# Kernel tuning notes

Measured on AMD Instinct MI355X. Metric: run time of the kernel, lower is better.

Reference implementation:

```python
import jax, jax.numpy as jnp
import numpy as np

N = 50000      # nodes
E = 800000     # random edges (self-loops appended -> E + N total)
IN = 128       # in_channels
H = 1          # heads
C = 128        # out_channels per head
NEG_SLOPE = 0.2


def setup_inputs() -> dict:
    key = jax.random.key(0)
    k1, k2, k3, k4, k5 = jax.random.split(key, 5)
    x = jax.random.normal(k1, (N, IN), jnp.float32)
    src = jax.random.randint(k2, (E,), 0, N)
    dst = jax.random.randint(k3, (E,), 0, N)
    loops = jnp.arange(N)
    # PyG 1.3.2 GATConv adds self-loops before propagate
    edge_index = jnp.stack([jnp.concatenate([src, loops]),
                            jnp.concatenate([dst, loops])]).astype(jnp.int64)
    W = jax.random.normal(k4, (IN, H * C), jnp.float32) * np.float32(1.0 / np.sqrt(IN))
    att = jax.random.normal(k5, (H, 2 * C), jnp.float32) * np.float32(0.1)
    bias = jnp.zeros((H * C,), jnp.float32)
    return {"x": x, "edge_index": edge_index, "W": W, "att": att, "bias": bias}


def reference(x, edge_index, W, att, bias):
    h = (x @ W).reshape(-1, H, C)            # [N,H,C] transformed features
    src, dst = edge_index[0], edge_index[1]  # j -> i
    hi = h[dst]                              # [Etot,H,C] x_i gather
    hj = h[src]                              # [Etot,H,C] x_j gather
    # alpha = sum(cat(x_i,x_j) * att, -1)
    alpha = (jnp.einsum('ehc,hc->eh', hi, att[:, :C])
             + jnp.einsum('ehc,hc->eh', hj, att[:, C:]))
    alpha = jax.nn.leaky_relu(alpha, NEG_SLOPE)
    # segment softmax over destination node (stable)
    m = jax.ops.segment_max(alpha, dst, num_segments=N)
    m = jnp.where(jnp.isfinite(m), m, 0.0)   # guard empty segments
    a = jnp.exp(alpha - m[dst])
    s = jax.ops.segment_sum(a, dst, num_segments=N)
    a = a / (s[dst] + 1e-16)
    # weighted scatter-add aggregation
    out = jax.ops.segment_sum(hj * a[:, :, None], dst, num_segments=N)  # [N,H,C]
    return out.reshape(-1, H * C) + bias
```

## Files before the change

kernel.cpp:

```cpp
#include <hip/hip_runtime.h>
#include <math.h>


constexpr int CH = 128;
constexpr int BNODES = 64;
constexpr int CAP = 2048;
constexpr int SCAP = 2560;
constexpr int NBMAX = 1024;
constexpr int SCHUNK = 8192;
constexpr int WTS = 136;
constexpr unsigned SENT = 0xFFFFFFFFu;

typedef __attribute__((ext_vector_type(8))) short bf16x8;
typedef __attribute__((ext_vector_type(4))) float f32x4;

static __device__ __forceinline__ unsigned short f2bf(float f) {
    unsigned u = __float_as_uint(f);
    unsigned r = (u + 0x7fffu + ((u >> 16) & 1u)) >> 16;
    return (unsigned short)r;
}

__global__ __launch_bounds__(256) void zero_kernel(int* __restrict__ p, int n) {
    int i = blockIdx.x * blockDim.x + threadIdx.x;
    if (i < n) p[i] = 0;
}

__global__ __launch_bounds__(256) void wt_kernel(const float* __restrict__ W,
                                                 unsigned short* __restrict__ WT) {
    const int T = blockIdx.x * 256 + threadIdx.x;
    const int k = T >> 4;
    const int n8 = (T & 15) * 8;
    const float4 a = *(const float4*)&W[k * CH + n8];
    const float4 b = *(const float4*)&W[k * CH + n8 + 4];
    WT[(n8 + 0) * WTS + k] = f2bf(a.x);
    WT[(n8 + 1) * WTS + k] = f2bf(a.y);
    WT[(n8 + 2) * WTS + k] = f2bf(a.z);
    WT[(n8 + 3) * WTS + k] = f2bf(a.w);
    WT[(n8 + 4) * WTS + k] = f2bf(b.x);
    WT[(n8 + 5) * WTS + k] = f2bf(b.y);
    WT[(n8 + 6) * WTS + k] = f2bf(b.z);
    WT[(n8 + 7) * WTS + k] = f2bf(b.w);
}

__global__ __launch_bounds__(256) void gemm_kernel(const float* __restrict__ x,
                                                   const unsigned short* __restrict__ WT,
                                                   const float* __restrict__ att,
                                                   unsigned short* __restrict__ hb,
                                                   float* __restrict__ ad,
                                                   float* __restrict__ as_, int n) {
    __shared__ unsigned short Wl[CH * WTS];
    const int tid = threadIdx.x;
    {
        const uint4* s = (const uint4*)WT;
        uint4* d = (uint4*)Wl;
        for (int i = tid; i < CH * WTS / 8; i += 256) d[i] = s[i];
    }
    __syncthreads();

    const int lane = tid & 63, wave = tid >> 6;
    const int m = lane & 15, quad = lane >> 4;
    const int row0 = blockIdx.x * 64 + wave * 16;
    const int row = min(row0 + m, n - 1);
    const float* xr = x + (size_t)row * CH;

    float4 a0[4], a1[4];
    #pragma unroll
    for (int t = 0; t < 4; ++t) {
        const int k0 = t * 32 + quad * 8;
        a0[t] = *(const float4*)&xr[k0];
        a1[t] = *(const float4*)&xr[k0 + 4];
    }
    bf16x8 afr[4];
    #pragma unroll
    for (int t = 0; t < 4; ++t) {
        afr[t][0] = (short)f2bf(a0[t].x); afr[t][1] = (short)f2bf(a0[t].y);
        afr[t][2] = (short)f2bf(a0[t].z); afr[t][3] = (short)f2bf(a0[t].w);
        afr[t][4] = (short)f2bf(a1[t].x); afr[t][5] = (short)f2bf(a1[t].y);
        afr[t][6] = (short)f2bf(a1[t].z); afr[t][7] = (short)f2bf(a1[t].w);
    }

    f32x4 acc[8] = {};
    #pragma unroll
    for (int t = 0; t < 4; ++t) {
        const int kb = t * 32 + quad * 8;
        #pragma unroll
        for (int nt = 0; nt < 8; ++nt) {
            const bf16x8 bfr = *(const bf16x8*)&Wl[(nt * 16 + m) * WTS + kb];
            acc[nt] = __builtin_amdgcn_mfma_f32_16x16x32_bf16(afr[t], bfr, acc[nt], 0, 0, 0);
        }
    }

    const int rbase = row0 + quad * 4;
    float pd[4] = {}, ps[4] = {};
    #pragma unroll
    for (int nt = 0; nt < 8; ++nt) {
        const int col = nt * 16 + m;
        const float atd = att[col], ats = att[CH + col];
        #pragma unroll
        for (int r = 0; r < 4; ++r) {
            pd[r] = fmaf(acc[nt][r], atd, pd[r]);
            ps[r] = fmaf(acc[nt][r], ats, ps[r]);
            const int rr = rbase + r;
            if (rr < n) hb[(size_t)rr * CH + col] = f2bf(acc[nt][r]);
        }
    }
    #pragma unroll
    for (int r = 0; r < 4; ++r) {
        #pragma unroll
        for (int off = 8; off >= 1; off >>= 1) {
            pd[r] += __shfl_xor(pd[r], off, 64);
            ps[r] += __shfl_xor(ps[r], off, 64);
        }
        const int rr = rbase + r;
        if (m == 0 && rr < n) { ad[rr] = pd[r]; as_[rr] = ps[r]; }
    }
}

__global__ __launch_bounds__(256) void scatter_kernel(const int* __restrict__ src,
                                                      const int* __restrict__ dst,
                                                      int* __restrict__ gcur,
                                                      unsigned* __restrict__ recs,
                                                      int etot, int nb) {
    __shared__ int hist[NBMAX];
    __shared__ int cur[NBMAX];
    __shared__ unsigned rbuf[SCHUNK];
    const int tid = threadIdx.x;
    const int e0 = blockIdx.x * SCHUNK;
    for (int t = tid; t < nb; t += 256) hist[t] = 0;
    __syncthreads();
    for (int i = tid; i < SCHUNK; i += 256) {
        const int e = e0 + i;
        if (e < etot) {
            const int d = dst[e];
            rbuf[i] = ((unsigned)d << 16) | (unsigned)src[e];
            atomicAdd(&hist[d >> 6], 1);
        }
    }
    __syncthreads();
    for (int t = tid; t < nb; t += 256) {
        const int h = hist[t];
        cur[t] = h ? atomicAdd(&gcur[t], h) : 0;
    }
    __syncthreads();
    for (int i = tid; i < SCHUNK; i += 256) {
        const int e = e0 + i;
        if (e < etot) {
            const unsigned r = rbuf[i];
            const int d = (int)(r >> 16);
            const int b = d >> 6;
            const int pos = atomicAdd(&cur[b], 1);
            if (pos < CAP)
                recs[(size_t)b * CAP + pos] = ((unsigned)(d & 63) << 16) | (r & 0xffffu);
        }
    }
}

__global__ __launch_bounds__(512) void aggregate_kernel(const unsigned char* __restrict__ hwb,
                                                        const float* __restrict__ ad,
                                                        const float* __restrict__ as_,
                                                        const int* __restrict__ gcur,
                                                        const unsigned* __restrict__ recs,
                                                        const float* __restrict__ bias,
                                                        float* __restrict__ out, int n) {
    __shared__ alignas(16) unsigned sorted[SCAP];
    __shared__ alignas(16) float alphas[SCAP];
    __shared__ int cnt[BNODES], ofs[BNODES], cur[BNODES];
    __shared__ int nEp_s;
    const int b = blockIdx.x;
    const int tid = threadIdx.x, lane = tid & 63, wid = tid >> 6;
    const unsigned* br = recs + (size_t)b * CAP;
    int nE = gcur[b]; if (nE > CAP) nE = CAP;
    unsigned* stash = (unsigned*)alphas;

    if (tid < BNODES) cnt[tid] = 0;
    __syncthreads();
    for (int i = tid; i < nE; i += 512) {
        const unsigned r = br[i];
        stash[i] = r;
        atomicAdd(&cnt[r >> 16], 1);
    }
    __syncthreads();
    if (wid == 0) {
        const int c = cnt[lane];
        const int cr = (c + 7) & ~7;
        int v = cr;
        #pragma unroll
        for (int off = 1; off < 64; off <<= 1) {
            const int u = __shfl_up(v, (unsigned)off, 64);
            if (lane >= off) v += u;
        }
        ofs[lane] = v - cr;
        cur[lane] = v - cr;
        if (lane == 63) nEp_s = v;
    }
    __syncthreads();
    const int nEp = nEp_s;
    for (int i = tid; i < nEp; i += 512) sorted[i] = SENT;
    __syncthreads();
    for (int i = tid; i < nE; i += 512) {
        const unsigned r = stash[i];
        const int pos = atomicAdd(&cur[r >> 16], 1);
        sorted[pos] = r;
    }
    __syncthreads();
    const float* adb = ad + b * BNODES;
    for (int i = tid; i < nEp; i += 512) {
        const unsigned r = sorted[i];
        float a = -3.0e38f;
        if (r != SENT) {
            a = adb[r >> 16] + as_[r & 0xffffu];
            a = (a >= 0.f) ? a : 0.2f * a;
        }
        alphas[i] = a;
    }
    __syncthreads();

    const unsigned lane4 = (unsigned)lane * 4u;
    for (int ln = wid; ln < BNODES; ln += 8) {
        const int node = b * BNODES + ln;
        if (node >= n) break;
        const int start = ofs[ln];
        const int endp = start + ((cnt[ln] + 7) & ~7);

        float m = -3.0e38f;
        for (int e = start + lane; e < endp; e += 64) m = fmaxf(m, alphas[e]);
        #pragma unroll
        for (int off = 32; off >= 1; off >>= 1) m = fmaxf(m, __shfl_xor(m, off, 64));

        float s = 0.f;
        for (int e = start + lane; e < endp; e += 64) {
            const float p = __expf(alphas[e] - m);
            alphas[e] = p;
            s += p;
            const unsigned r = sorted[e];
            sorted[e] = (r == SENT) ? 0u : ((r & 0xffffu) << 8);
        }
        #pragma unroll
        for (int off = 32; off >= 1; off >>= 1) s += __shfl_xor(s, off, 64);

        float acc0 = 0.f, acc1 = 0.f;
        for (int e = start; e < endp; e += 8) {
            const uint4 sa = *(const uint4*)&sorted[e];
            const uint4 sb = *(const uint4*)&sorted[e + 4];
            const float4 pa = *(const float4*)&alphas[e];
            const float4 pb = *(const float4*)&alphas[e + 4];
            const unsigned g0 = *(const unsigned*)(hwb + (sa.x + lane4));
            const unsigned g1 = *(const unsigned*)(hwb + (sa.y + lane4));
            const unsigned g2 = *(const unsigned*)(hwb + (sa.z + lane4));
            const unsigned g3 = *(const unsigned*)(hwb + (sa.w + lane4));
            const unsigned g4 = *(const unsigned*)(hwb + (sb.x + lane4));
            const unsigned g5 = *(const unsigned*)(hwb + (sb.y + lane4));
            const unsigned g6 = *(const unsigned*)(hwb + (sb.z + lane4));
            const unsigned g7 = *(const unsigned*)(hwb + (sb.w + lane4));
            acc0 = fmaf(pa.x, __uint_as_float((g0 & 0xffffu) << 16), acc0);
            acc1 = fmaf(pa.x, __uint_as_float(g0 & 0xffff0000u), acc1);
            acc0 = fmaf(pa.y, __uint_as_float((g1 & 0xffffu) << 16), acc0);
            acc1 = fmaf(pa.y, __uint_as_float(g1 & 0xffff0000u), acc1);
            acc0 = fmaf(pa.z, __uint_as_float((g2 & 0xffffu) << 16), acc0);
            acc1 = fmaf(pa.z, __uint_as_float(g2 & 0xffff0000u), acc1);
            acc0 = fmaf(pa.w, __uint_as_float((g3 & 0xffffu) << 16), acc0);
            acc1 = fmaf(pa.w, __uint_as_float(g3 & 0xffff0000u), acc1);
            acc0 = fmaf(pb.x, __uint_as_float((g4 & 0xffffu) << 16), acc0);
            acc1 = fmaf(pb.x, __uint_as_float(g4 & 0xffff0000u), acc1);
            acc0 = fmaf(pb.y, __uint_as_float((g5 & 0xffffu) << 16), acc0);
            acc1 = fmaf(pb.y, __uint_as_float(g5 & 0xffff0000u), acc1);
            acc0 = fmaf(pb.z, __uint_as_float((g6 & 0xffffu) << 16), acc0);
            acc1 = fmaf(pb.z, __uint_as_float(g6 & 0xffff0000u), acc1);
            acc0 = fmaf(pb.w, __uint_as_float((g7 & 0xffffu) << 16), acc0);
            acc1 = fmaf(pb.w, __uint_as_float(g7 & 0xffff0000u), acc1);
        }
        const float inv = 1.f / (s + 1e-16f);
        const float2 bv = *(const float2*)&bias[lane * 2];
        float2 o;
        o.x = fmaf(acc0, inv, bv.x);
        o.y = fmaf(acc1, inv, bv.y);
        *(float2*)&out[node * CH + lane * 2] = o;
    }
}

extern "C" void kernel_launch(void* const* d_in, const int* in_sizes, int n_in,
                              void* d_out, int out_size, void* d_ws, size_t ws_size,
                              hipStream_t stream) {
    const float* x    = (const float*)d_in[0];
    const int*   ei   = (const int*)d_in[1];
    const float* W    = (const float*)d_in[2];
    const float* att  = (const float*)d_in[3];
    const float* bias = (const float*)d_in[4];
    float* out = (float*)d_out;

    const int N_   = in_sizes[0] / CH;
    const int Etot = in_sizes[1] / 2;
    const int* src = ei;
    const int* dst = ei + Etot;
    const int nb = (N_ + BNODES - 1) / BNODES;

    char* ws = (char*)d_ws;
    size_t off = 0;
    auto alloc = [&](size_t bytes) -> void* {
        void* p = ws + off;
        off = (off + bytes + 255) & ~(size_t)255;
        return p;
    };
    unsigned short* hb = (unsigned short*)alloc((size_t)N_ * CH * sizeof(unsigned short));
    unsigned short* WT = (unsigned short*)alloc((size_t)CH * WTS * sizeof(unsigned short));
    float* ad      = (float*)alloc((size_t)N_ * sizeof(float));
    float* as_     = (float*)alloc((size_t)N_ * sizeof(float));
    int*   gcur    = (int*)  alloc((size_t)nb * sizeof(int));
    unsigned* recs = (unsigned*)alloc((size_t)nb * CAP * sizeof(unsigned));
    (void)ws_size; (void)n_in; (void)out_size;

    zero_kernel<<<(nb + 255) / 256, 256, 0, stream>>>(gcur, nb);
    wt_kernel<<<8, 256, 0, stream>>>(W, WT);
    gemm_kernel<<<(N_ + 63) / 64, 256, 0, stream>>>(x, WT, att, hb, ad, as_, N_);
    scatter_kernel<<<(Etot + SCHUNK - 1) / SCHUNK, 256, 0, stream>>>(src, dst, gcur, recs, Etot, nb);
    aggregate_kernel<<<nb, 512, 0, stream>>>((const unsigned char*)hb, ad, as_, gcur, recs, bias, out, N_);
}
```

Measured before the change: 153.1 us.

## Fuse zero into transpose kernel and run GEMM and scatter in one launch

Zeroing of the bucket counters moves into the weight-transpose kernel, and the GEMM and edge-scatter kernels are merged into one launch where block index selects the role. This removes two kernel launches and lets the independent GEMM and scatter work run concurrently on the GPU instead of back to back. The aggregate kernel also caches the per-block destination attention scores in shared memory. The cost is a shared 40 KB LDS allocation for every block, which can lower occupancy for the GEMM blocks. Correctness relies on the transpose grid covering all counters (8*256 >= nb).

Measured after the change: 144.5 us. 1.06x faster.

```diff
diff --git a/kernel.cpp b/kernel.cpp
--- a/kernel.cpp
+++ b/kernel.cpp
@@ -20,14 +20,11 @@
     return (unsigned short)r;
 }
 
-__global__ __launch_bounds__(256) void zero_kernel(int* __restrict__ p, int n) {
-    int i = blockIdx.x * blockDim.x + threadIdx.x;
-    if (i < n) p[i] = 0;
-}
-
-__global__ __launch_bounds__(256) void wt_kernel(const float* __restrict__ W,
-                                                 unsigned short* __restrict__ WT) {
+__global__ __launch_bounds__(256) void wtzero_kernel(const float* __restrict__ W,
+                                                     unsigned short* __restrict__ WT,
+                                                     int* __restrict__ gcur, int nb) {
     const int T = blockIdx.x * 256 + threadIdx.x;
+    if (T < nb) gcur[T] = 0;
     const int k = T >> 4;
     const int n8 = (T & 15) * 8;
     const float4 a = *(const float4*)&W[k * CH + n8];
@@ -42,115 +39,117 @@
     WT[(n8 + 7) * WTS + k] = f2bf(b.w);
 }
 
-__global__ __launch_bounds__(256) void gemm_kernel(const float* __restrict__ x,
-                                                   const unsigned short* __restrict__ WT,
-                                                   const float* __restrict__ att,
-                                                   unsigned short* __restrict__ hb,
-                                                   float* __restrict__ ad,
-                                                   float* __restrict__ as_, int n) {
-    __shared__ unsigned short Wl[CH * WTS];
+__global__ __launch_bounds__(256) void gemm_scatter_kernel(const float* __restrict__ x,
+                                                           const unsigned short* __restrict__ WT,
+                                                           const float* __restrict__ att,
+                                                           unsigned short* __restrict__ hb,
+                                                           float* __restrict__ ad,
+                                                           float* __restrict__ as_,
+                                                           const int* __restrict__ src,
+                                                           const int* __restrict__ dst,
+                                                           int* __restrict__ gcur,
+                                                           unsigned* __restrict__ recs,
+                                                           int n, int etot, int nb, int gb) {
+    __shared__ alignas(16) unsigned char smem[40960];
     const int tid = threadIdx.x;
-    {
-        const uint4* s = (const uint4*)WT;
-        uint4* d = (uint4*)Wl;
-        for (int i = tid; i < CH * WTS / 8; i += 256) d[i] = s[i];
-    }
-    __syncthreads();
-
-    const int lane = tid & 63, wave = tid >> 6;
-    const int m = lane & 15, quad = lane >> 4;
-    const int row0 = blockIdx.x * 64 + wave * 16;
-    const int row = min(row0 + m, n - 1);
-    const float* xr = x + (size_t)row * CH;
-
-    float4 a0[4], a1[4];
-    #pragma unroll
-    for (int t = 0; t < 4; ++t) {
-        const int k0 = t * 32 + quad * 8;
-        a0[t] = *(const float4*)&xr[k0];
-        a1[t] = *(const float4*)&xr[k0 + 4];
-    }
-    bf16x8 afr[4];
-    #pragma unroll
-    for (int t = 0; t < 4; ++t) {
-        afr[t][0] = (short)f2bf(a0[t].x); afr[t][1] = (short)f2bf(a0[t].y);
-        afr[t][2] = (short)f2bf(a0[t].z); afr[t][3] = (short)f2bf(a0[t].w);
-        afr[t][4] = (short)f2bf(a1[t].x); afr[t][5] = (short)f2bf(a1[t].y);
-        afr[t][6] = (short)f2bf(a1[t].z); afr[t][7] = (short)f2bf(a1[t].w);
-    }
-
-    f32x4 acc[8] = {};
-    #pragma unroll
-    for (int t = 0; t < 4; ++t) {
-        const int kb = t * 32 + quad * 8;
+
+    if ((int)blockIdx.x < gb) {
+        unsigned short* Wl = (unsigned short*)smem;
+        {
+            const uint4* s = (const uint4*)WT;
+            uint4* d = (uint4*)Wl;
+            for (int i = tid; i < CH * WTS / 8; i += 256) d[i] = s[i];
+        }
+        __syncthreads();
+
+        const int lane = tid & 63, wave = tid >> 6;
+        const int m = lane & 15, quad = lane >> 4;
+        const int row0 = blockIdx.x * 64 + wave * 16;
+        const int row = min(row0 + m, n - 1);
+        const float* xr = x + (size_t)row * CH;
+
+        float4 a0[4], a1[4];
+        #pragma unroll
+        for (int t = 0; t < 4; ++t) {
+            const int k0 = t * 32 + quad * 8;
+            a0[t] = *(const float4*)&xr[k0];
+            a1[t] = *(const float4*)&xr[k0 + 4];
+        }
+        bf16x8 afr[4];
+        #pragma unroll
+        for (int t = 0; t < 4; ++t) {
+            afr[t][0] = (short)f2bf(a0[t].x); afr[t][1] = (short)f2bf(a0[t].y);
+            afr[t][2] = (short)f2bf(a0[t].z); afr[t][3] = (short)f2bf(a0[t].w);
+            afr[t][4] = (short)f2bf(a1[t].x); afr[t][5] = (short)f2bf(a1[t].y);
+            afr[t][6] = (short)f2bf(a1[t].z); afr[t][7] = (short)f2bf(a1[t].w);
+        }
+
+        f32x4 acc[8] = {};
+        #pragma unroll
+        for (int t = 0; t < 4; ++t) {
+            const int kb = t * 32 + quad * 8;
+            #pragma unroll
+            for (int nt = 0; nt < 8; ++nt) {
+                const bf16x8 bfr = *(const bf16x8*)&Wl[(nt * 16 + m) * WTS + kb];
+                acc[nt] = __builtin_amdgcn_mfma_f32_16x16x32_bf16(afr[t], bfr, acc[nt], 0, 0, 0);
+            }
+        }
+
+        const int rbase = row0 + quad * 4;
+        float pd[4] = {}, ps[4] = {};
         #pragma unroll
         for (int nt = 0; nt < 8; ++nt) {
-            const bf16x8 bfr = *(const bf16x8*)&Wl[(nt * 16 + m) * WTS + kb];
-            acc[nt] = __builtin_amdgcn_mfma_f32_16x16x32_bf16(afr[t], bfr, acc[nt], 0, 0, 0);
-        }
-    }
-
-    const int rbase = row0 + quad * 4;
-    float pd[4] = {}, ps[4] = {};
-    #pragma unroll
-    for (int nt = 0; nt < 8; ++nt) {
-        const int col = nt * 16 + m;
-        const float atd = att[col], ats = att[CH + col];
+            const int col = nt * 16 + m;
+            const float atd = att[col], ats = att[CH + col];
+            #pragma unroll
+            for (int r = 0; r < 4; ++r) {
+                pd[r] = fmaf(acc[nt][r], atd, pd[r]);
+                ps[r] = fmaf(acc[nt][r], ats, ps[r]);
+                const int rr = rbase + r;
+                if (rr < n) hb[(size_t)rr * CH + col] = f2bf(acc[nt][r]);
+            }
+        }
         #pragma unroll
         for (int r = 0; r < 4; ++r) {
-            pd[r] = fmaf(acc[nt][r], atd, pd[r]);
-            ps[r] = fmaf(acc[nt][r], ats, ps[r]);
+            #pragma unroll
+            for (int off = 8; off >= 1; off >>= 1) {
+                pd[r] += __shfl_xor(pd[r], off, 64);
+                ps[r] += __shfl_xor(ps[r], off, 64);
+            }
             const int rr = rbase + r;
-            if (rr < n) hb[(size_t)rr * CH + col] = f2bf(acc[nt][r]);
-        }
-    }
-    #pragma unroll
-    for (int r = 0; r < 4; ++r) {
-        #pragma unroll
-        for (int off = 8; off >= 1; off >>= 1) {
-            pd[r] += __shfl_xor(pd[r], off, 64);
-            ps[r] += __shfl_xor(ps[r], off, 64);
-        }
-        const int rr = rbase + r;
-        if (m == 0 && rr < n) { ad[rr] = pd[r]; as_[rr] = ps[r]; }
-    }
-}
-
-__global__ __launch_bounds__(256) void scatter_kernel(const int* __restrict__ src,
-                                                      const int* __restrict__ dst,
-                                                      int* __restrict__ gcur,
-                                                      unsigned* __restrict__ recs,
-                                                      int etot, int nb) {
-    __shared__ int hist[NBMAX];
-    __shared__ int cur[NBMAX];
-    __shared__ unsigned rbuf[SCHUNK];
-    const int tid = threadIdx.x;
-    const int e0 = blockIdx.x * SCHUNK;
-    for (int t = tid; t < nb; t += 256) hist[t] = 0;
-    __syncthreads();
-    for (int i = tid; i < SCHUNK; i += 256) {
-        const int e = e0 + i;
-        if (e < etot) {
-            const int d = dst[e];
-            rbuf[i] = ((unsigned)d << 16) | (unsigned)src[e];
-            atomicAdd(&hist[d >> 6], 1);
-        }
-    }
-    __syncthreads();
-    for (int t = tid; t < nb; t += 256) {
-        const int h = hist[t];
-        cur[t] = h ? atomicAdd(&gcur[t], h) : 0;
-    }
-    __syncthreads();
-    for (int i = tid; i < SCHUNK; i += 256) {
-        const int e = e0 + i;
-        if (e < etot) {
-            const unsigned r = rbuf[i];
-            const int d = (int)(r >> 16);
-            const int b = d >> 6;
-            const int pos = atomicAdd(&cur[b], 1);
-            if (pos < CAP)
-                recs[(size_t)b * CAP + pos] = ((unsigned)(d & 63) << 16) | (r & 0xffffu);
+            if (m == 0 && rr < n) { ad[rr] = pd[r]; as_[rr] = ps[r]; }
+        }
+    } else {
+        int* hist = (int*)smem;
+        int* cur = hist + NBMAX;
+        unsigned* rbuf = (unsigned*)(cur + NBMAX);
+        const int e0 = ((int)blockIdx.x - gb) * SCHUNK;
+        for (int t = tid; t < nb; t += 256) hist[t] = 0;
+        __syncthreads();
+        for (int i = tid; i < SCHUNK; i += 256) {
+            const int e = e0 + i;
+            if (e < etot) {
+                const int d = dst[e];
+                rbuf[i] = ((unsigned)d << 16) | (unsigned)src[e];
+                atomicAdd(&hist[d >> 6], 1);
+            }
+        }
+        __syncthreads();
+        for (int t = tid; t < nb; t += 256) {
+            const int h = hist[t];
+            cur[t] = h ? atomicAdd(&gcur[t], h) : 0;
+        }
+        __syncthreads();
+        for (int i = tid; i < SCHUNK; i += 256) {
+            const int e = e0 + i;
+            if (e < etot) {
+                const unsigned r = rbuf[i];
+                const int d = (int)(r >> 16);
+                const int b = d >> 6;
+                const int pos = atomicAdd(&cur[b], 1);
+                if (pos < CAP)
+                    recs[(size_t)b * CAP + pos] = ((unsigned)(d & 63) << 16) | (r & 0xffffu);
+            }
         }
     }
 }
@@ -164,6 +163,7 @@
                                                         float* __restrict__ out, int n) {
     __shared__ alignas(16) unsigned sorted[SCAP];
     __shared__ alignas(16) float alphas[SCAP];
+    __shared__ float adl[BNODES];
     __shared__ int cnt[BNODES], ofs[BNODES], cur[BNODES];
     __shared__ int nEp_s;
     const int b = blockIdx.x;
@@ -172,7 +172,11 @@
     int nE = gcur[b]; if (nE > CAP) nE = CAP;
     unsigned* stash = (unsigned*)alphas;
 
-    if (tid < BNODES) cnt[tid] = 0;
+    if (tid < BNODES) {
+        cnt[tid] = 0;
+        const int node = b * BNODES + tid;
+        adl[tid] = (node < n) ? ad[node] : 0.f;
+    }
     __syncthreads();
     for (int i = tid; i < nE; i += 512) {
         const unsigned r = br[i];
@@ -203,12 +207,11 @@
         sorted[pos] = r;
     }
     __syncthreads();
-    const float* adb = ad + b * BNODES;
     for (int i = tid; i < nEp; i += 512) {
         const unsigned r = sorted[i];
         float a = -3.0e38f;
         if (r != SENT) {
-            a = adb[r >> 16] + as_[r & 0xffffu];
+            a = adl[r >> 16] + as_[r & 0xffffu];
             a = (a >= 0.f) ? a : 0.2f * a;
         }
         alphas[i] = a;
@@ -293,6 +296,8 @@
     const int* src = ei;
     const int* dst = ei + Etot;
     const int nb = (N_ + BNODES - 1) / BNODES;
+    const int gb = (N_ + 63) / 64;
+    const int sb = (Etot + SCHUNK - 1) / SCHUNK;
 
     char* ws = (char*)d_ws;
     size_t off = 0;
@@ -309,9 +314,8 @@
     unsigned* recs = (unsigned*)alloc((size_t)nb * CAP * sizeof(unsigned));
     (void)ws_size; (void)n_in; (void)out_size;
 
-    zero_kernel<<<(nb + 255) / 256, 256, 0, stream>>>(gcur, nb);
-    wt_kernel<<<8, 256, 0, stream>>>(W, WT);
-    gemm_kernel<<<(N_ + 63) / 64, 256, 0, stream>>>(x, WT, att, hb, ad, as_, N_);
-    scatter_kernel<<<(Etot + SCHUNK - 1) / SCHUNK, 256, 0, stream>>>(src, dst, gcur, recs, Etot, nb);
+    wtzero_kernel<<<8, 256, 0, stream>>>(W, WT, gcur, nb);
+    gemm_scatter_kernel<<<gb + sb, 256, 0, stream>>>(x, WT, att, hb, ad, as_,
+                                                     src, dst, gcur, recs, N_, Etot, nb, gb);
     aggregate_kernel<<<nb, 512, 0, stream>>>((const unsigned char*)hb, ad, as_, gcur, recs, bias, out, N_);
 }
```
